# Kernel optimization log

Hardware: AMD Instinct MI355X
Metric: run time of the kernel (lower is better)

The kernel has to match this reference:

```python
import jax, jax.numpy as jnp
import numpy as np

C = 512
NUM_HEADS = 8


def setup_inputs() -> dict:
    key = jax.random.key(0)
    k1, k2, k3 = jax.random.split(key, 3)
    x = jax.random.normal(k1, (16, C, 32, 32), dtype=jnp.float32)
    # torch Linear(C, 3C) weight shape [3C, C]; y = x @ W.T
    w_qkv = jax.random.normal(k2, (3 * C, C), dtype=jnp.float32) * (1.0 / np.sqrt(C))
    w_out = jax.random.normal(k3, (C, C), dtype=jnp.float32) * (1.0 / np.sqrt(C))
    return {"x": x, "w_qkv": w_qkv, "w_out": w_out}


def reference(x, w_qkv, w_out):
    B, Cc, H, W = x.shape
    S = H * W
    hd = Cc // NUM_HEADS
    # NCHW -> (B, S, C)
    xs = jnp.transpose(x, (0, 2, 3, 1)).reshape(B, S, Cc)
    qkv = jnp.einsum('bsc,dc->bsd', xs, w_qkv).reshape(B, S, 3, NUM_HEADS, hd)
    q = jnp.transpose(qkv[:, :, 0], (0, 2, 1, 3))  # (B, h, S, hd)
    k = jnp.transpose(qkv[:, :, 1], (0, 2, 1, 3))
    v = jnp.transpose(qkv[:, :, 2], (0, 2, 1, 3))
    scale = 1.0 / np.sqrt(hd)
    logits = jnp.einsum('bhqd,bhkd->bhqk', q, k) * scale
    attn = jax.nn.softmax(logits, axis=-1)
    o = jnp.einsum('bhqk,bhkd->bhqd', attn, v)  # (B, h, S, hd)
    o = jnp.transpose(o, (0, 2, 1, 3)).reshape(B, S, Cc)
    out = jnp.einsum('bsc,dc->bsd', o, w_out)
    return jnp.transpose(out.reshape(B, H, W, Cc), (0, 3, 1, 2))
```

## Files before the change

### kernel.cpp

```cpp
#include <hip/hip_runtime.h>
#include <hip/hip_bf16.h>
#include <stdint.h>


typedef __bf16 bf16x8 __attribute__((ext_vector_type(8)));
typedef __bf16 bf16x4 __attribute__((ext_vector_type(4)));
typedef float  f32x4  __attribute__((ext_vector_type(4)));
typedef short  s16x4  __attribute__((ext_vector_type(4)));

#if __has_builtin(__builtin_amdgcn_exp2f)
#define EXP2(x) __builtin_amdgcn_exp2f(x)
#else
#define EXP2(x) exp2f(x)
#endif

#define GLDS16(gptr, lptr)                                                        \
  __builtin_amdgcn_global_load_lds(                                               \
      (const __attribute__((address_space(1))) uint32_t*)(gptr),                  \
      (__attribute__((address_space(3))) uint32_t*)(lptr), 16, 0, 0)

__global__ __launch_bounds__(256) void k_transpose_x(const float* __restrict__ x,
                                                     __bf16* __restrict__ xs) {
  __shared__ float tl[64][36];
  const int s0 = blockIdx.x * 32, c0 = blockIdx.y * 64, b = blockIdx.z;
  const int t = threadIdx.x;
  const int cl = t >> 2, f0 = (t & 3) * 2;
#pragma unroll
  for (int i = 0; i < 2; ++i) {
    const float4 v = *reinterpret_cast<const float4*>(
        x + ((size_t)(b * 512 + c0 + cl)) * 1024 + s0 + (f0 + i) * 4);
    *reinterpret_cast<float4*>(&tl[cl][(f0 + i) * 4]) = v;
  }
  __syncthreads();
  const int sl = t >> 3, ch = t & 7;
  bf16x8 o;
#pragma unroll
  for (int j = 0; j < 8; ++j) o[j] = (__bf16)tl[ch * 8 + j][sl];
  *reinterpret_cast<bf16x8*>(xs + ((size_t)(b * 1024 + s0 + sl)) * 512 + c0 + ch * 8) = o;
}

__global__ __launch_bounds__(256) void k_cast_w(const float* __restrict__ wqkv,
                                                const float* __restrict__ wout,
                                                __bf16* __restrict__ wqkvb,
                                                __bf16* __restrict__ woutb) {
  const int blk = blockIdx.x;
  const float* in = (blk < 768) ? wqkv : wout;
  __bf16* out = (blk < 768) ? wqkvb : woutb;
  const int i = ((blk < 768) ? blk : blk - 768) * 256 + threadIdx.x;
  const float4 v = reinterpret_cast<const float4*>(in)[i];
  bf16x4 o = {(__bf16)v.x, (__bf16)v.y, (__bf16)v.z, (__bf16)v.w};
  reinterpret_cast<bf16x4*>(out)[i] = o;
}

__device__ __forceinline__ void gemm_core(const __bf16* __restrict__ Ag,
                                          const __bf16* __restrict__ Bg,
                                          int m0, int n0,
                                          __bf16* As, __bf16* Bs,
                                          f32x4 (&acc)[4][4]) {
  const int tid = threadIdx.x, lane = tid & 63, wv = tid >> 6;
  const int wm = (wv >> 1) * 64, wn = (wv & 1) * 64;
  const int lr = lane & 15, lq = lane >> 4;
  const int srl = lane >> 2, pc = lane & 3;
  const int gcs = ((pc ^ (srl & 3)) * 8);

#define GSTAGE(k0s, buf)                                                           \
  {                                                                                \
    _Pragma("unroll") for (int t = 0; t < 2; ++t) {                                \
      const int r0 = wv * 32 + t * 16;                                             \
      const int sr = r0 + srl;                                                     \
      GLDS16(Ag + (size_t)(m0 + sr) * 512 + (k0s) + gcs, &As[(buf) * 4096 + r0 * 32]); \
      GLDS16(Bg + (size_t)(n0 + sr) * 512 + (k0s) + gcs, &Bs[(buf) * 4096 + r0 * 32]); \
    }                                                                              \
  }

  GSTAGE(0, 0);
  __syncthreads();
#pragma unroll 2
  for (int k0 = 0; k0 < 512; k0 += 32) {
    const int cur = (k0 >> 5) & 1;
    if (k0 < 480) GSTAGE(k0 + 32, cur ^ 1);
    bf16x8 af[4], bfr[4];
#pragma unroll
    for (int i = 0; i < 4; ++i) {
      const int row = wm + i * 16 + lr;
      af[i] = *reinterpret_cast<const bf16x8*>(
          &As[cur * 4096 + row * 32 + ((lq ^ (lr & 3)) * 8)]);
    }
#pragma unroll
    for (int j = 0; j < 4; ++j) {
      const int row = wn + j * 16 + lr;
      bfr[j] = *reinterpret_cast<const bf16x8*>(
          &Bs[cur * 4096 + row * 32 + ((lq ^ (lr & 3)) * 8)]);
    }
#pragma unroll
    for (int i = 0; i < 4; ++i)
#pragma unroll
      for (int j = 0; j < 4; ++j)
        acc[i][j] = __builtin_amdgcn_mfma_f32_16x16x32_bf16(af[i], bfr[j], acc[i][j], 0, 0, 0);
    __syncthreads();
  }
#undef GSTAGE
}

__global__ __launch_bounds__(256, 4) void k_qkv_gemm(const __bf16* __restrict__ xs,
                                                     const __bf16* __restrict__ wq,
                                                     __bf16* __restrict__ Q,
                                                     __bf16* __restrict__ K,
                                                     __bf16* __restrict__ Vt) {
  __shared__ __align__(16) __bf16 As[2 * 128 * 32];
  __shared__ __align__(16) __bf16 Bs[2 * 128 * 32];
  const int m0 = blockIdx.x * 128, n0 = blockIdx.y * 128;
  const int tid = threadIdx.x, lane = tid & 63, wv = tid >> 6;
  const int wm = (wv >> 1) * 64, wn = (wv & 1) * 64;
  const int lr = lane & 15, lq = lane >> 4;
  f32x4 acc[4][4] = {};
  gemm_core(xs, wq, m0, n0, As, Bs, acc);
  const float QSC = 0.125f * 1.44269504088896341f;
#pragma unroll
  for (int i = 0; i < 4; ++i) {
    const int mg0 = m0 + wm + i * 16 + lq * 4;
    const int b = mg0 >> 10, s = mg0 & 1023;
#pragma unroll
    for (int j = 0; j < 4; ++j) {
      const int ng = n0 + wn + j * 16 + lr;
      const int t = ng >> 9, h = (ng >> 6) & 7, d = ng & 63;
      if (t == 0) {
#pragma unroll
        for (int r = 0; r < 4; ++r)
          Q[((size_t)((b * 8 + h) * 1024 + s + r)) * 64 + d] = (__bf16)(acc[i][j][r] * QSC);
      } else if (t == 1) {
#pragma unroll
        for (int r = 0; r < 4; ++r)
          K[((size_t)((b * 8 + h) * 1024 + s + r)) * 64 + d] = (__bf16)acc[i][j][r];
      } else {
        bf16x4 pv = {(__bf16)acc[i][j][0], (__bf16)acc[i][j][1],
                     (__bf16)acc[i][j][2], (__bf16)acc[i][j][3]};
        *reinterpret_cast<bf16x4*>(&Vt[((size_t)((b * 8 + h) * 64 + d)) * 1024 + s]) = pv;
      }
    }
  }
}

__global__ __launch_bounds__(256, 4) void k_attn(const __bf16* __restrict__ Q,
                                                 const __bf16* __restrict__ K,
                                                 const __bf16* __restrict__ Vt,
                                                 __bf16* __restrict__ O) {
  __shared__ __align__(16) __bf16 Ks[2][64 * 64];
  __shared__ __align__(16) __bf16 Vs[2][64 * 64];
  const int bh = blockIdx.x & 127, qt = blockIdx.x >> 7;
  const int b = bh >> 3, h = bh & 7;
  const int tid = threadIdx.x, lane = tid & 63, wv = tid >> 6;
  const int lr = lane & 15, lq = lane >> 4;
  const size_t hbase = (size_t)bh * 65536;

  bf16x8 qb[2][2];
#pragma unroll
  for (int g = 0; g < 2; ++g)
#pragma unroll
    for (int kx = 0; kx < 2; ++kx)
      qb[g][kx] = *reinterpret_cast<const bf16x8*>(
          Q + hbase + (size_t)(qt * 128 + wv * 32 + g * 16 + lr) * 64 + kx * 32 + lq * 8);

  const int srow8 = lane >> 3, sc = lane & 7;
  int srow[2], sgc[2];
#pragma unroll
  for (int t = 0; t < 2; ++t) {
    srow[t] = wv * 16 + t * 8 + srow8;
    sgc[t] = ((sc ^ (srow[t] & 7)) * 8);
  }
#define STAGE(kt, buf)                                                             \
  {                                                                                \
    _Pragma("unroll") for (int t = 0; t < 2; ++t) {                                \
      const int r0 = wv * 16 + t * 8;                                              \
      GLDS16(K + hbase + (size_t)((kt) * 64 + srow[t]) * 64 + sgc[t],              \
             &Ks[buf][r0 * 64]);                                                   \
      GLDS16(Vt + hbase + (size_t)srow[t] * 1024 + (kt) * 64 + sgc[t],             \
             &Vs[buf][r0 * 64]);                                                   \
    }                                                                              \
  }

  float l_run[2] = {0.f, 0.f};
  f32x4 o_acc[2][4] = {};

  STAGE(0, 0);
  __syncthreads();

#pragma unroll 2
  for (int kt = 0; kt < 16; ++kt) {
    const int cur = kt & 1;
    if (kt < 15) STAGE(kt + 1, cur ^ 1);
    f32x4 sacc[2][4] = {};
#pragma unroll
    for (int kx = 0; kx < 2; ++kx)
#pragma unroll
      for (int jt = 0; jt < 4; ++jt) {
        const int row = jt * 16 + lr;
        const bf16x8 ka = *reinterpret_cast<const bf16x8*>(
            &Ks[cur][row * 64 + (((kx * 4 + lq) ^ (lr & 7)) * 8)]);
        sacc[0][jt] = __builtin_amdgcn_mfma_f32_16x16x32_bf16(ka, qb[0][kx], sacc[0][jt], 0, 0, 0);
        sacc[1][jt] = __builtin_amdgcn_mfma_f32_16x16x32_bf16(ka, qb[1][kx], sacc[1][jt], 0, 0, 0);
      }
    s16x4 pb[2][4];
#pragma unroll
    for (int g = 0; g < 2; ++g) {
      float ls = 0.f;
#pragma unroll
      for (int c = 0; c < 4; ++c) {
        const float p0 = EXP2(sacc[g][c][0]);
        const float p1 = EXP2(sacc[g][c][1]);
        const float p2 = EXP2(sacc[g][c][2]);
        const float p3 = EXP2(sacc[g][c][3]);
        ls += (p0 + p1) + (p2 + p3);
        bf16x4 pv = {(__bf16)p0, (__bf16)p1, (__bf16)p2, (__bf16)p3};
        pb[g][c] = __builtin_bit_cast(s16x4, pv);
      }
      l_run[g] += ls;
    }
#pragma unroll
    for (int c = 0; c < 4; ++c)
#pragma unroll
      for (int dt = 0; dt < 4; ++dt) {
        const int d = dt * 16 + lr;
        const s16x4 va = *reinterpret_cast<const s16x4*>(
            &Vs[cur][d * 64 + (((2 * c + (lq >> 1)) ^ (lr & 7)) * 8) + (lq & 1) * 4]);
        o_acc[0][dt] = __builtin_amdgcn_mfma_f32_16x16x16bf16_1k(va, pb[0][c], o_acc[0][dt], 0, 0, 0);
        o_acc[1][dt] = __builtin_amdgcn_mfma_f32_16x16x16bf16_1k(va, pb[1][c], o_acc[1][dt], 0, 0, 0);
      }
    __syncthreads();
  }
#pragma unroll
  for (int g = 0; g < 2; ++g) {
    float l1 = l_run[g] + __shfl_xor(l_run[g], 16, 64);
    const float inv = 1.0f / (l1 + __shfl_xor(l1, 32, 64));
    const int sg = qt * 128 + wv * 32 + g * 16 + lr;
#pragma unroll
    for (int dt = 0; dt < 4; ++dt) {
      const int c0 = h * 64 + dt * 16 + lq * 4;
      bf16x4 ov = {(__bf16)(o_acc[g][dt][0] * inv), (__bf16)(o_acc[g][dt][1] * inv),
                   (__bf16)(o_acc[g][dt][2] * inv), (__bf16)(o_acc[g][dt][3] * inv)};
      *reinterpret_cast<bf16x4*>(&O[((size_t)(b * 1024 + sg)) * 512 + c0]) = ov;
    }
  }
}

__global__ __launch_bounds__(256, 4) void k_out_gemm(const __bf16* __restrict__ wo,
                                                     const __bf16* __restrict__ Ob,
                                                     float* __restrict__ out) {
  __shared__ __align__(16) __bf16 As[2 * 128 * 32];
  __shared__ __align__(16) __bf16 Bs[2 * 128 * 32];
  const int n0 = blockIdx.x * 128, m0 = blockIdx.y * 128;
  const int tid = threadIdx.x, lane = tid & 63, wv = tid >> 6;
  const int wm = (wv >> 1) * 64, wn = (wv & 1) * 64;
  const int lr = lane & 15, lq = lane >> 4;
  f32x4 acc[4][4] = {};
  gemm_core(wo, Ob, m0, n0, As, Bs, acc);
  const int b = n0 >> 10;
#pragma unroll
  for (int i = 0; i < 4; ++i) {
    const int cch = m0 + wm + i * 16 + lq * 4;
#pragma unroll
    for (int j = 0; j < 4; ++j) {
      const int s = (n0 & 1023) + wn + j * 16 + lr;
#pragma unroll
      for (int r = 0; r < 4; ++r)
        out[((size_t)(b * 512 + cch + r)) * 1024 + s] = acc[i][j][r];
    }
  }
}

extern "C" void kernel_launch(void* const* d_in, const int* in_sizes, int n_in,
                              void* d_out, int out_size, void* d_ws, size_t ws_size,
                              hipStream_t stream) {
  const float* x    = (const float*)d_in[0];
  const float* wqkv = (const float*)d_in[1];
  const float* wout = (const float*)d_in[2];
  float* out = (float*)d_out;
  char* ws = (char*)d_ws;
  __bf16* xs    = (__bf16*)(ws);
  __bf16* wqkvb = (__bf16*)(ws + 16777216);
  __bf16* woutb = (__bf16*)(ws + 18350080);
  __bf16* Qb    = (__bf16*)(ws + 18874368);
  __bf16* Kb    = (__bf16*)(ws + 35651584);
  __bf16* Vtb   = (__bf16*)(ws + 52428800);
  __bf16* Ob    = (__bf16*)(ws + 69206016);

  k_transpose_x<<<dim3(32, 8, 16), dim3(256), 0, stream>>>(x, xs);
  k_cast_w<<<dim3(1024), dim3(256), 0, stream>>>(wqkv, wout, wqkvb, woutb);
  k_qkv_gemm<<<dim3(128, 12), dim3(256), 0, stream>>>(xs, wqkvb, Qb, Kb, Vtb);
  k_attn<<<dim3(1024), dim3(256), 0, stream>>>(Qb, Kb, Vtb, Ob);
  k_out_gemm<<<dim3(128, 4), dim3(256), 0, stream>>>(woutb, Ob, out);
}
```

Before: 194.4 us.

## Fuse prep kernels, halve attention and output-GEMM tiles for more blocks

Merges the x transpose and the weight cast into one launch by giving the cast its own z-slices of the grid, which removes one kernel launch. Each attention block now handles 64 queries instead of 128, so the grid doubles to 2048 blocks. The output GEMM uses 64x128 tiles instead of 128x128, also doubling its block count. The aim is better occupancy and load balance across CUs, at the price of loading each K/V and B tile twice as often and running fewer MFMAs per LDS read.

Result: faster. 186.5 us (-4.0%).

```diff
diff --git a/kernel.cpp b/kernel.cpp
--- a/kernel.cpp
+++ b/kernel.cpp
@@ -19,11 +19,26 @@
       (const __attribute__((address_space(1))) uint32_t*)(gptr),                  \
       (__attribute__((address_space(3))) uint32_t*)(lptr), 16, 0, 0)
 
-__global__ __launch_bounds__(256) void k_transpose_x(const float* __restrict__ x,
-                                                     __bf16* __restrict__ xs) {
+__global__ __launch_bounds__(256) void k_prep(const float* __restrict__ x,
+                                              __bf16* __restrict__ xs,
+                                              const float* __restrict__ wqkv,
+                                              const float* __restrict__ wout,
+                                              __bf16* __restrict__ wqkvb,
+                                              __bf16* __restrict__ woutb) {
+  const int z = blockIdx.z;
+  const int t = threadIdx.x;
+  if (z >= 16) {
+    const int cid = (z - 16) * 256 + blockIdx.y * 32 + blockIdx.x;
+    const float* in = (cid < 768) ? wqkv : wout;
+    __bf16* out = (cid < 768) ? wqkvb : woutb;
+    const int i = ((cid < 768) ? cid : cid - 768) * 256 + t;
+    const float4 v = reinterpret_cast<const float4*>(in)[i];
+    bf16x4 o = {(__bf16)v.x, (__bf16)v.y, (__bf16)v.z, (__bf16)v.w};
+    reinterpret_cast<bf16x4*>(out)[i] = o;
+    return;
+  }
   __shared__ float tl[64][36];
-  const int s0 = blockIdx.x * 32, c0 = blockIdx.y * 64, b = blockIdx.z;
-  const int t = threadIdx.x;
+  const int s0 = blockIdx.x * 32, c0 = blockIdx.y * 64, b = z;
   const int cl = t >> 2, f0 = (t & 3) * 2;
 #pragma unroll
   for (int i = 0; i < 2; ++i) {
@@ -37,19 +52,6 @@
 #pragma unroll
   for (int j = 0; j < 8; ++j) o[j] = (__bf16)tl[ch * 8 + j][sl];
   *reinterpret_cast<bf16x8*>(xs + ((size_t)(b * 1024 + s0 + sl)) * 512 + c0 + ch * 8) = o;
-}
-
-__global__ __launch_bounds__(256) void k_cast_w(const float* __restrict__ wqkv,
-                                                const float* __restrict__ wout,
-                                                __bf16* __restrict__ wqkvb,
-                                                __bf16* __restrict__ woutb) {
-  const int blk = blockIdx.x;
-  const float* in = (blk < 768) ? wqkv : wout;
-  __bf16* out = (blk < 768) ? wqkvb : woutb;
-  const int i = ((blk < 768) ? blk : blk - 768) * 256 + threadIdx.x;
-  const float4 v = reinterpret_cast<const float4*>(in)[i];
-  bf16x4 o = {(__bf16)v.x, (__bf16)v.y, (__bf16)v.z, (__bf16)v.w};
-  reinterpret_cast<bf16x4*>(out)[i] = o;
 }
 
 __device__ __forceinline__ void gemm_core(const __bf16* __restrict__ Ag,
@@ -153,13 +155,11 @@
   const int lr = lane & 15, lq = lane >> 4;
   const size_t hbase = (size_t)bh * 65536;
 
-  bf16x8 qb[2][2];
-#pragma unroll
-  for (int g = 0; g < 2; ++g)
-#pragma unroll
-    for (int kx = 0; kx < 2; ++kx)
-      qb[g][kx] = *reinterpret_cast<const bf16x8*>(
-          Q + hbase + (size_t)(qt * 128 + wv * 32 + g * 16 + lr) * 64 + kx * 32 + lq * 8);
+  bf16x8 qb[2];
+#pragma unroll
+  for (int kx = 0; kx < 2; ++kx)
+    qb[kx] = *reinterpret_cast<const bf16x8*>(
+        Q + hbase + (size_t)(qt * 64 + wv * 16 + lr) * 64 + kx * 32 + lq * 8);
 
   const int srow8 = lane >> 3, sc = lane & 7;
   int srow[2], sgc[2];
@@ -179,8 +179,8 @@
     }                                                                              \
   }
 
-  float l_run[2] = {0.f, 0.f};
-  f32x4 o_acc[2][4] = {};
+  float l_run = 0.f;
+  f32x4 o_acc[4] = {};
 
   STAGE(0, 0);
   __syncthreads();
@@ -189,77 +189,107 @@
   for (int kt = 0; kt < 16; ++kt) {
     const int cur = kt & 1;
     if (kt < 15) STAGE(kt + 1, cur ^ 1);
-    f32x4 sacc[2][4] = {};
+    f32x4 sacc[4] = {};
 #pragma unroll
     for (int kx = 0; kx < 2; ++kx)
 #pragma unroll
       for (int jt = 0; jt < 4; ++jt) {
-        const int row = jt * 16 + lr;
         const bf16x8 ka = *reinterpret_cast<const bf16x8*>(
-            &Ks[cur][row * 64 + (((kx * 4 + lq) ^ (lr & 7)) * 8)]);
-        sacc[0][jt] = __builtin_amdgcn_mfma_f32_16x16x32_bf16(ka, qb[0][kx], sacc[0][jt], 0, 0, 0);
-        sacc[1][jt] = __builtin_amdgcn_mfma_f32_16x16x32_bf16(ka, qb[1][kx], sacc[1][jt], 0, 0, 0);
+            &Ks[cur][(jt * 16 + lr) * 64 + (((kx * 4 + lq) ^ (lr & 7)) * 8)]);
+        sacc[jt] = __builtin_amdgcn_mfma_f32_16x16x32_bf16(ka, qb[kx], sacc[jt], 0, 0, 0);
       }
-    s16x4 pb[2][4];
-#pragma unroll
-    for (int g = 0; g < 2; ++g) {
-      float ls = 0.f;
-#pragma unroll
-      for (int c = 0; c < 4; ++c) {
-        const float p0 = EXP2(sacc[g][c][0]);
-        const float p1 = EXP2(sacc[g][c][1]);
-        const float p2 = EXP2(sacc[g][c][2]);
-        const float p3 = EXP2(sacc[g][c][3]);
-        ls += (p0 + p1) + (p2 + p3);
-        bf16x4 pv = {(__bf16)p0, (__bf16)p1, (__bf16)p2, (__bf16)p3};
-        pb[g][c] = __builtin_bit_cast(s16x4, pv);
-      }
-      l_run[g] += ls;
-    }
+    s16x4 pb[4];
+    float ls = 0.f;
+#pragma unroll
+    for (int c = 0; c < 4; ++c) {
+      const float p0 = EXP2(sacc[c][0]);
+      const float p1 = EXP2(sacc[c][1]);
+      const float p2 = EXP2(sacc[c][2]);
+      const float p3 = EXP2(sacc[c][3]);
+      ls += (p0 + p1) + (p2 + p3);
+      bf16x4 pv = {(__bf16)p0, (__bf16)p1, (__bf16)p2, (__bf16)p3};
+      pb[c] = __builtin_bit_cast(s16x4, pv);
+    }
+    l_run += ls;
 #pragma unroll
     for (int c = 0; c < 4; ++c)
 #pragma unroll
       for (int dt = 0; dt < 4; ++dt) {
-        const int d = dt * 16 + lr;
         const s16x4 va = *reinterpret_cast<const s16x4*>(
-            &Vs[cur][d * 64 + (((2 * c + (lq >> 1)) ^ (lr & 7)) * 8) + (lq & 1) * 4]);
-        o_acc[0][dt] = __builtin_amdgcn_mfma_f32_16x16x16bf16_1k(va, pb[0][c], o_acc[0][dt], 0, 0, 0);
-        o_acc[1][dt] = __builtin_amdgcn_mfma_f32_16x16x16bf16_1k(va, pb[1][c], o_acc[1][dt], 0, 0, 0);
+            &Vs[cur][(dt * 16 + lr) * 64 + (((2 * c + (lq >> 1)) ^ (lr & 7)) * 8) + (lq & 1) * 4]);
+        o_acc[dt] = __builtin_amdgcn_mfma_f32_16x16x16bf16_1k(va, pb[c], o_acc[dt], 0, 0, 0);
       }
     __syncthreads();
   }
-#pragma unroll
-  for (int g = 0; g < 2; ++g) {
-    float l1 = l_run[g] + __shfl_xor(l_run[g], 16, 64);
-    const float inv = 1.0f / (l1 + __shfl_xor(l1, 32, 64));
-    const int sg = qt * 128 + wv * 32 + g * 16 + lr;
-#pragma unroll
-    for (int dt = 0; dt < 4; ++dt) {
-      const int c0 = h * 64 + dt * 16 + lq * 4;
-      bf16x4 ov = {(__bf16)(o_acc[g][dt][0] * inv), (__bf16)(o_acc[g][dt][1] * inv),
-                   (__bf16)(o_acc[g][dt][2] * inv), (__bf16)(o_acc[g][dt][3] * inv)};
-      *reinterpret_cast<bf16x4*>(&O[((size_t)(b * 1024 + sg)) * 512 + c0]) = ov;
-    }
+  float l1 = l_run + __shfl_xor(l_run, 16, 64);
+  const float inv = 1.0f / (l1 + __shfl_xor(l1, 32, 64));
+  const int sg = qt * 64 + wv * 16 + lr;
+#pragma unroll
+  for (int dt = 0; dt < 4; ++dt) {
+    const int c0 = h * 64 + dt * 16 + lq * 4;
+    bf16x4 ov = {(__bf16)(o_acc[dt][0] * inv), (__bf16)(o_acc[dt][1] * inv),
+                 (__bf16)(o_acc[dt][2] * inv), (__bf16)(o_acc[dt][3] * inv)};
+    *reinterpret_cast<bf16x4*>(&O[((size_t)(b * 1024 + sg)) * 512 + c0]) = ov;
   }
 }
 
 __global__ __launch_bounds__(256, 4) void k_out_gemm(const __bf16* __restrict__ wo,
                                                      const __bf16* __restrict__ Ob,
                                                      float* __restrict__ out) {
-  __shared__ __align__(16) __bf16 As[2 * 128 * 32];
+  __shared__ __align__(16) __bf16 As[2 * 64 * 32];
   __shared__ __align__(16) __bf16 Bs[2 * 128 * 32];
-  const int n0 = blockIdx.x * 128, m0 = blockIdx.y * 128;
+  const int n0 = blockIdx.x * 128, m0 = blockIdx.y * 64;
   const int tid = threadIdx.x, lane = tid & 63, wv = tid >> 6;
-  const int wm = (wv >> 1) * 64, wn = (wv & 1) * 64;
+  const int wn = wv * 32;
   const int lr = lane & 15, lq = lane >> 4;
-  f32x4 acc[4][4] = {};
-  gemm_core(wo, Ob, m0, n0, As, Bs, acc);
+  const int srl = lane >> 2, pc = lane & 3;
+  const int gcs = ((pc ^ (srl & 3)) * 8);
+  f32x4 acc[4][2] = {};
+
+#define OSTAGE(k0s, buf)                                                           \
+  {                                                                                \
+    const int ra = wv * 16 + srl;                             \
+    GLDS16(wo + (size_t)(m0 + ra) * 512 + (k0s) + gcs, &As[(buf) * 2048 + wv * 512]); \
+    _Pragma("unroll") for (int t = 0; t < 2; ++t) {                                \
+      const int r0 = wv * 32 + t * 16;                                             \
+      const int rb = r0 + srl;                                                     \
+      GLDS16(Ob + (size_t)(n0 + rb) * 512 + (k0s) + gcs, &Bs[(buf) * 4096 + r0 * 32]); \
+    }                                                                              \
+  }
+
+  OSTAGE(0, 0);
+  __syncthreads();
+#pragma unroll 2
+  for (int k0 = 0; k0 < 512; k0 += 32) {
+    const int cur = (k0 >> 5) & 1;
+    if (k0 < 480) OSTAGE(k0 + 32, cur ^ 1);
+    bf16x8 af[4], bfr[2];
+#pragma unroll
+    for (int i = 0; i < 4; ++i) {
+      const int row = i * 16 + lr;
+      af[i] = *reinterpret_cast<const bf16x8*>(
+          &As[cur * 2048 + row * 32 + ((lq ^ (lr & 3)) * 8)]);
+    }
+#pragma unroll
+    for (int j = 0; j < 2; ++j) {
+      const int row = wn + j * 16 + lr;
+      bfr[j] = *reinterpret_cast<const bf16x8*>(
+          &Bs[cur * 4096 + row * 32 + ((lq ^ (lr & 3)) * 8)]);
+    }
+#pragma unroll
+    for (int i = 0; i < 4; ++i)
+#pragma unroll
+      for (int j = 0; j < 2; ++j)
+        acc[i][j] = __builtin_amdgcn_mfma_f32_16x16x32_bf16(af[i], bfr[j], acc[i][j], 0, 0, 0);
+    __syncthreads();
+  }
+#undef OSTAGE
   const int b = n0 >> 10;
 #pragma unroll
   for (int i = 0; i < 4; ++i) {
-    const int cch = m0 + wm + i * 16 + lq * 4;
-#pragma unroll
-    for (int j = 0; j < 4; ++j) {
+    const int cch = m0 + i * 16 + lq * 4;
+#pragma unroll
+    for (int j = 0; j < 2; ++j) {
       const int s = (n0 & 1023) + wn + j * 16 + lr;
 #pragma unroll
       for (int r = 0; r < 4; ++r)
@@ -284,9 +314,8 @@
   __bf16* Vtb   = (__bf16*)(ws + 52428800);
   __bf16* Ob    = (__bf16*)(ws + 69206016);
 
-  k_transpose_x<<<dim3(32, 8, 16), dim3(256), 0, stream>>>(x, xs);
-  k_cast_w<<<dim3(1024), dim3(256), 0, stream>>>(wqkv, wout, wqkvb, woutb);
+  k_prep<<<dim3(32, 8, 20), dim3(256), 0, stream>>>(x, xs, wqkv, wout, wqkvb, woutb);
   k_qkv_gemm<<<dim3(128, 12), dim3(256), 0, stream>>>(xs, wqkvb, Qb, Kb, Vtb);
-  k_attn<<<dim3(1024), dim3(256), 0, stream>>>(Qb, Kb, Vtb, Ob);
-  k_out_gemm<<<dim3(128, 4), dim3(256), 0, stream>>>(woutb, Ob, out);
-}
+  k_attn<<<dim3(2048), dim3(256), 0, stream>>>(Qb, Kb, Vtb, Ob);
+  k_out_gemm<<<dim3(128, 8), dim3(256), 0, stream>>>(woutb, Ob, out);
+}
```
